# Optimization experiments

Hardware: AMD Instinct MI355X
Metric: run time of the kernel (lower is better)

The kernel has to match this reference:

```python
import jax, jax.numpy as jnp
import numpy as np

D = 512          # input_size (feature dim)
C = 100          # num_classes
N = 2048         # test samples
ALPHA = 0.5      # regularization mixing parameter
SHRINK = 1e-4    # shrinkage_param


def setup_inputs() -> dict:
    key = jax.random.key(0)
    k1, k2, k3, k4, k5 = jax.random.split(key, 5)
    X = jax.random.normal(k1, (N, D), dtype=jnp.float32)
    muK = jax.random.normal(k2, (C, D), dtype=jnp.float32)
    # Per-class covariances: PSD, well-conditioned (like fitted streaming covariances)
    A = jax.random.normal(k3, (C, D, D), dtype=jnp.float32) * 0.05
    SigmaK = jnp.einsum('cij,ckj->cik', A, A) + 0.1 * jnp.eye(D, dtype=jnp.float32)
    B = jax.random.normal(k4, (D, D), dtype=jnp.float32) * 0.05
    Sigma = B @ B.T + 0.1 * jnp.eye(D, dtype=jnp.float32)
    # class counts (all > 0 so every class is active)
    cK = jax.random.uniform(k5, (C,), dtype=jnp.float32, minval=1.0, maxval=1000.0)
    return {"X": X, "muK": muK, "SigmaK": SigmaK, "Sigma": Sigma, "cK": cK}


def reference(X, muK, SigmaK, Sigma, cK):
    # RegSigmaK[k] = alpha * SigmaK[k] + (1-alpha) * Sigma           [C, D, D]
    RegSigmaK = ALPHA * SigmaK + (1.0 - ALPHA) * Sigma[None, :, :]
    # priors (classes with zero count get prior 1, then are masked to -inf below)
    s = jnp.sum(cK)
    prior = jnp.where(cK == 0, 1.0, cK / s)                          # [C]
    # Lambda[k] = pinv((1-sh) * RegSigmaK[k] + sh * I)               [C, D, D]
    eye = jnp.eye(D, dtype=RegSigmaK.dtype)
    Lambda = jnp.linalg.pinv((1.0 - SHRINK) * RegSigmaK + SHRINK * eye)
    # 0.5 * log ||RegSigmaK[k]||_F  (torch.norm default = Frobenius)
    half_lognorm = 0.5 * jnp.log(jnp.linalg.norm(RegSigmaK, axis=(1, 2)))  # [C]
    # batched Mahalanobis quadratic form: (x - mu_k)^T Lambda_k (x - mu_k)
    diff = X[:, None, :] - muK[None, :, :]                           # [N, C, D]
    quad = jnp.einsum('ncd,cde,nce->nc', diff, Lambda, diff)         # [N, C]
    scores = jnp.log(prior)[None, :] - half_lognorm[None, :] - 0.5 * quad
    scores = jnp.where((cK == 0)[None, :], -jnp.inf, scores)
    return scores
```

## Files before the change

### kernel.cpp

```cpp
#include <hip/hip_runtime.h>
#include <math.h>

#define DIM 512
#define NCLS 100
#define NS 2048
#define DD (DIM*DIM)
#define SHRINKV 1e-4f

typedef short bf16x8 __attribute__((ext_vector_type(8)));
typedef short s16x4 __attribute__((ext_vector_type(4)));
typedef float f32x4 __attribute__((ext_vector_type(4)));

static __device__ __forceinline__ short f2bf(float f) {
  unsigned int u = __float_as_uint(f);
  u += 0x7FFFu + ((u >> 16) & 1u);
  return (short)(u >> 16);
}

__global__ __launch_bounds__(256) void prep_kernel(const float* __restrict__ SigmaK,
                                                   const float* __restrict__ Sigma,
                                                   float* __restrict__ M,
                                                   float* __restrict__ aux) {
  int b = blockIdx.x;
  int k = b >> 2, chunk = b & 3;
  const float* Sk = SigmaK + (size_t)k * DD;
  float* Mk = M + (size_t)k * DD;
  int base0 = chunk << 16;
  float fro = 0.f;
  const float oms = 1.0f - SHRINKV;
  for (int it = 0; it < 64; ++it) {
    int idx = base0 + (it << 10) + (threadIdx.x << 2);
    float4 a = *(const float4*)(Sk + idx);
    float4 g = *(const float4*)(Sigma + idx);
    int r = idx >> 9, c = idx & 511;
    float4 reg;
    reg.x = 0.5f*(a.x + g.x); reg.y = 0.5f*(a.y + g.y);
    reg.z = 0.5f*(a.z + g.z); reg.w = 0.5f*(a.w + g.w);
    fro += reg.x*reg.x + reg.y*reg.y + reg.z*reg.z + reg.w*reg.w;
    float4 m;
    m.x = oms*reg.x + ((r == c + 0) ? SHRINKV : 0.f);
    m.y = oms*reg.y + ((r == c + 1) ? SHRINKV : 0.f);
    m.z = oms*reg.z + ((r == c + 2) ? SHRINKV : 0.f);
    m.w = oms*reg.w + ((r == c + 3) ? SHRINKV : 0.f);
    *(float4*)(Mk + idx) = m;
  }
  __shared__ float red[4];
  int lane = threadIdx.x & 63, w = threadIdx.x >> 6;
  for (int o = 32; o > 0; o >>= 1) fro += __shfl_down(fro, o);
  if (lane == 0) red[w] = fro;
  __syncthreads();
  if (threadIdx.x == 0) atomicAdd(&aux[1 + k], red[0] + red[1] + red[2] + red[3]);
}

__global__ __launch_bounds__(256) void fdt_kernel(float* __restrict__ M,
                                                  short* __restrict__ Wb, int p) {
  __shared__ float Llds[64 * 68];
  __shared__ float invT[64 * 68];
  __shared__ float TA[64 * 68];
  int kcls = blockIdx.x;
  float* Mk = M + (size_t)kcls * DD;
  short* Wk = Wb + (size_t)kcls * DD;
  int tid = threadIdx.x, lane = tid & 63, wv = tid >> 6;
  int ty = tid >> 4, tx = tid & 15;
  int sr = tid >> 2, sq = (tid & 3) << 4;
  int p0 = p << 6;
  if (wv == 0) {
    float row[64];
    const float* src = Mk + (size_t)(p0 + lane) * DIM + p0;
    #pragma unroll
    for (int c4 = 0; c4 < 64; c4 += 4) {
      float4 v = *(const float4*)(src + c4);
      row[c4] = v.x; row[c4+1] = v.y; row[c4+2] = v.z; row[c4+3] = v.w;
    }
    #pragma unroll
    for (int j = 0; j < 64; ++j) {
      float diagv = __shfl(row[j], j);
      float dv = sqrtf(diagv);
      float rinv = 1.0f / dv;
      float myLj = row[j] * rinv;
      row[j] = myLj;
      #pragma unroll
      for (int c = j + 1; c < 64; ++c)
        row[c] = fmaf(-myLj, __shfl(myLj, c), row[c]);
    }
    #pragma unroll
    for (int c = 0; c < 64; ++c)
      Llds[lane * 68 + c] = (c <= lane) ? row[c] : 0.f;
  }
  __syncthreads();
  if (wv == 0) {
    float w[64];
    #pragma unroll
    for (int r = 0; r < 64; ++r) {
      float s = 0.f;
      #pragma unroll
      for (int kk = 0; kk + 4 <= r; kk += 4) {
        float4 lv = *(const float4*)(Llds + r*68 + kk);
        s += lv.x*w[kk] + lv.y*w[kk+1] + lv.z*w[kk+2] + lv.w*w[kk+3];
      }
      #pragma unroll
      for (int kk = r & ~3; kk < r; ++kk) s += Llds[r*68 + kk] * w[kk];
      float rhs = ((r == lane) ? 1.0f : 0.0f) - s;
      w[r] = rhs / Llds[r*68 + r];
    }
    #pragma unroll
    for (int r = 0; r < 64; ++r) {
      Mk[(size_t)(p0 + r)*DIM + p0 + lane] = w[r];
      Wk[(size_t)(p0 + r)*DIM + p0 + lane] = f2bf(w[r]);
      invT[lane*68 + r] = w[r];
    }
  }
  __syncthreads();
  for (int i = p + 1; i < 8; ++i) {
    {
      const float* a = Mk + (size_t)((i << 6) + sr)*DIM + p0 + sq;
      #pragma unroll
      for (int t4 = 0; t4 < 4; ++t4) {
        float4 va = *(const float4*)(a + 4*t4);
        TA[(sq+4*t4+0)*68+sr]=va.x; TA[(sq+4*t4+1)*68+sr]=va.y;
        TA[(sq+4*t4+2)*68+sr]=va.z; TA[(sq+4*t4+3)*68+sr]=va.w;
      }
    }
    __syncthreads();
    float acc[4][4];
    #pragma unroll
    for (int a2 = 0; a2 < 4; ++a2)
      #pragma unroll
      for (int b2 = 0; b2 < 4; ++b2) acc[a2][b2] = 0.f;
    #pragma unroll 16
    for (int m = 0; m < 64; ++m) {
      float4 av = *(const float4*)(TA + m*68 + (ty << 2));
      float4 bv = *(const float4*)(invT + m*68 + (tx << 2));
      float a4[4] = {av.x, av.y, av.z, av.w};
      float b4[4] = {bv.x, bv.y, bv.z, bv.w};
      #pragma unroll
      for (int ir = 0; ir < 4; ++ir)
        #pragma unroll
        for (int ic = 0; ic < 4; ++ic) acc[ir][ic] += a4[ir] * b4[ic];
    }
    #pragma unroll
    for (int q = 0; q < 4; ++q) {
      float4 v; v.x = acc[q][0]; v.y = acc[q][1]; v.z = acc[q][2]; v.w = acc[q][3];
      *(float4*)(Mk + (size_t)((i << 6) + (ty << 2) + q)*DIM + p0 + (tx << 2)) = v;
    }
    __syncthreads();
  }
}

__global__ __launch_bounds__(256) void syrk_kernel(float* __restrict__ M, int p) {
  __shared__ float TA[64 * 68];
  __shared__ float TB[64 * 68];
  int n = 7 - p;
  int T = n * (n + 1) / 2;
  int cls = blockIdx.x / T;
  int t = blockIdx.x % T;
  int bi = 0;
  while (t > bi) { t -= bi + 1; ++bi; }
  int i = p + 1 + bi, j = p + 1 + t;
  float* Mk = M + (size_t)cls * DD;
  int tid = threadIdx.x;
  int ty = tid >> 4, tx = tid & 15;
  int sr = tid >> 2, sq = (tid & 3) << 4;
  {
    const float* a = Mk + (size_t)((i << 6) + sr)*DIM + (p << 6) + sq;
    const float* b = Mk + (size_t)((j << 6) + sr)*DIM + (p << 6) + sq;
    #pragma unroll
    for (int t4 = 0; t4 < 4; ++t4) {
      float4 va = *(const float4*)(a + 4*t4);
      TA[(sq+4*t4+0)*68+sr]=va.x; TA[(sq+4*t4+1)*68+sr]=va.y;
      TA[(sq+4*t4+2)*68+sr]=va.z; TA[(sq+4*t4+3)*68+sr]=va.w;
      float4 vb = *(const float4*)(b + 4*t4);
      TB[(sq+4*t4+0)*68+sr]=vb.x; TB[(sq+4*t4+1)*68+sr]=vb.y;
      TB[(sq+4*t4+2)*68+sr]=vb.z; TB[(sq+4*t4+3)*68+sr]=vb.w;
    }
  }
  __syncthreads();
  float acc[4][4];
  #pragma unroll
  for (int a = 0; a < 4; ++a)
    #pragma unroll
    for (int b = 0; b < 4; ++b) acc[a][b] = 0.f;
  #pragma unroll 16
  for (int m = 0; m < 64; ++m) {
    float4 av = *(const float4*)(TA + m*68 + (ty << 2));
    float4 bv = *(const float4*)(TB + m*68 + (tx << 2));
    float a4[4] = {av.x, av.y, av.z, av.w};
    float b4[4] = {bv.x, bv.y, bv.z, bv.w};
    #pragma unroll
    for (int ir = 0; ir < 4; ++ir)
      #pragma unroll
      for (int ic = 0; ic < 4; ++ic) acc[ir][ic] += a4[ir] * b4[ic];
  }
  #pragma unroll
  for (int q = 0; q < 4; ++q) {
    float* dst = Mk + (size_t)((i << 6) + (ty << 2) + q)*DIM + (j << 6) + (tx << 2);
    float4 v = *(const float4*)dst;
    v.x -= acc[q][0]; v.y -= acc[q][1]; v.z -= acc[q][2]; v.w -= acc[q][3];
    *(float4*)dst = v;
  }
}

__global__ __launch_bounds__(256) void tail_kernel(float* __restrict__ M,
                                                   short* __restrict__ Wb) {
  __shared__ float Llds[64 * 68];
  __shared__ float invT[64 * 68];
  __shared__ float TA[64 * 68];
  __shared__ float TB[64 * 68];
  int kcls = blockIdx.x;
  float* Mk = M + (size_t)kcls * DD;
  short* Wk = Wb + (size_t)kcls * DD;
  int tid = threadIdx.x, lane = tid & 63, wv = tid >> 6;
  int ty = tid >> 4, tx = tid & 15;
  int sr = tid >> 2, sq = (tid & 3) << 4;
  for (int p = 4; p < 8; ++p) {
    int p0 = p << 6;
    __syncthreads();
    if (wv == 0) {
      float row[64];
      const float* src = Mk + (size_t)(p0 + lane) * DIM + p0;
      #pragma unroll
      for (int c4 = 0; c4 < 64; c4 += 4) {
        float4 v = *(const float4*)(src + c4);
        row[c4] = v.x; row[c4+1] = v.y; row[c4+2] = v.z; row[c4+3] = v.w;
      }
      #pragma unroll
      for (int j = 0; j < 64; ++j) {
        float diagv = __shfl(row[j], j);
        float dv = sqrtf(diagv);
        float rinv = 1.0f / dv;
        float myLj = row[j] * rinv;
        row[j] = myLj;
        #pragma unroll
        for (int c = j + 1; c < 64; ++c)
          row[c] = fmaf(-myLj, __shfl(myLj, c), row[c]);
      }
      #pragma unroll
      for (int c = 0; c < 64; ++c)
        Llds[lane * 68 + c] = (c <= lane) ? row[c] : 0.f;
    }
    __syncthreads();
    if (wv == 0) {
      float w[64];
      #pragma unroll
      for (int r = 0; r < 64; ++r) {
        float s = 0.f;
        #pragma unroll
        for (int kk = 0; kk + 4 <= r; kk += 4) {
          float4 lv = *(const float4*)(Llds + r*68 + kk);
          s += lv.x*w[kk] + lv.y*w[kk+1] + lv.z*w[kk+2] + lv.w*w[kk+3];
        }
        #pragma unroll
        for (int kk = r & ~3; kk < r; ++kk) s += Llds[r*68 + kk] * w[kk];
        float rhs = ((r == lane) ? 1.0f : 0.0f) - s;
        w[r] = rhs / Llds[r*68 + r];
      }
      #pragma unroll
      for (int r = 0; r < 64; ++r) {
        Mk[(size_t)(p0 + r)*DIM + p0 + lane] = w[r];
        Wk[(size_t)(p0 + r)*DIM + p0 + lane] = f2bf(w[r]);
        invT[lane*68 + r] = w[r];
      }
    }
    __syncthreads();
    for (int i = p + 1; i < 8; ++i) {
      {
        const float* a = Mk + (size_t)((i << 6) + sr)*DIM + p0 + sq;
        #pragma unroll
        for (int t4 = 0; t4 < 4; ++t4) {
          float4 va = *(const float4*)(a + 4*t4);
          TA[(sq+4*t4+0)*68+sr]=va.x; TA[(sq+4*t4+1)*68+sr]=va.y;
          TA[(sq+4*t4+2)*68+sr]=va.z; TA[(sq+4*t4+3)*68+sr]=va.w;
        }
      }
      __syncthreads();
      float acc[4][4];
      #pragma unroll
      for (int a2 = 0; a2 < 4; ++a2)
        #pragma unroll
        for (int b2 = 0; b2 < 4; ++b2) acc[a2][b2] = 0.f;
      #pragma unroll 16
      for (int m = 0; m < 64; ++m) {
        float4 av = *(const float4*)(TA + m*68 + (ty << 2));
        float4 bv = *(const float4*)(invT + m*68 + (tx << 2));
        float a4[4] = {av.x, av.y, av.z, av.w};
        float b4[4] = {bv.x, bv.y, bv.z, bv.w};
        #pragma unroll
        for (int ir = 0; ir < 4; ++ir)
          #pragma unroll
          for (int ic = 0; ic < 4; ++ic) acc[ir][ic] += a4[ir] * b4[ic];
      }
      #pragma unroll
      for (int q = 0; q < 4; ++q) {
        float4 v; v.x = acc[q][0]; v.y = acc[q][1]; v.z = acc[q][2]; v.w = acc[q][3];
        *(float4*)(Mk + (size_t)((i << 6) + (ty << 2) + q)*DIM + p0 + (tx << 2)) = v;
      }
      __syncthreads();
    }
    for (int i = p + 1; i < 8; ++i) {
      for (int j = p + 1; j <= i; ++j) {
        {
          const float* a = Mk + (size_t)((i << 6) + sr)*DIM + p0 + sq;
          const float* b = Mk + (size_t)((j << 6) + sr)*DIM + p0 + sq;
          #pragma unroll
          for (int t4 = 0; t4 < 4; ++t4) {
            float4 va = *(const float4*)(a + 4*t4);
            TA[(sq+4*t4+0)*68+sr]=va.x; TA[(sq+4*t4+1)*68+sr]=va.y;
            TA[(sq+4*t4+2)*68+sr]=va.z; TA[(sq+4*t4+3)*68+sr]=va.w;
            float4 vb = *(const float4*)(b + 4*t4);
            TB[(sq+4*t4+0)*68+sr]=vb.x; TB[(sq+4*t4+1)*68+sr]=vb.y;
            TB[(sq+4*t4+2)*68+sr]=vb.z; TB[(sq+4*t4+3)*68+sr]=vb.w;
          }
        }
        __syncthreads();
        float acc[4][4];
        #pragma unroll
        for (int a2 = 0; a2 < 4; ++a2)
          #pragma unroll
          for (int b2 = 0; b2 < 4; ++b2) acc[a2][b2] = 0.f;
        #pragma unroll 16
        for (int m = 0; m < 64; ++m) {
          float4 av = *(const float4*)(TA + m*68 + (ty << 2));
          float4 bv = *(const float4*)(TB + m*68 + (tx << 2));
          float a4[4] = {av.x, av.y, av.z, av.w};
          float b4[4] = {bv.x, bv.y, bv.z, bv.w};
          #pragma unroll
          for (int ir = 0; ir < 4; ++ir)
            #pragma unroll
            for (int ic = 0; ic < 4; ++ic) acc[ir][ic] += a4[ir] * b4[ic];
        }
        #pragma unroll
        for (int q = 0; q < 4; ++q) {
          float* dst = Mk + (size_t)((i << 6) + (ty << 2) + q)*DIM + (j << 6) + (tx << 2);
          float4 v = *(const float4*)dst;
          v.x -= acc[q][0]; v.y -= acc[q][1]; v.z -= acc[q][2]; v.w -= acc[q][3];
          *(float4*)dst = v;
        }
        __syncthreads();
      }
    }
  }
}

__global__ __launch_bounds__(256) void colsweep_kernel(float* __restrict__ M,
                                                       short* __restrict__ Wb) {
  __shared__ float TL[64 * 68];
  __shared__ float TW[64 * 68];
  int cls = blockIdx.x / 7;
  int j = blockIdx.x % 7;
  float* Mk = M + (size_t)cls * DD;
  short* Wk = Wb + (size_t)cls * DD;
  int tid = threadIdx.x;
  int ty = tid >> 4, tx = tid & 15;
  int sr = tid >> 2, sq = (tid & 3) << 4;
  for (int i = j + 1; i < 8; ++i) {
    float acc[4][4];
    #pragma unroll
    for (int a = 0; a < 4; ++a)
      #pragma unroll
      for (int b = 0; b < 4; ++b) acc[a][b] = 0.f;
    for (int k = j; k < i; ++k) {
      __syncthreads();
      {
        const float* a = Mk + (size_t)((i << 6) + sr)*DIM + (k << 6) + sq;
        const float* b = Mk + (size_t)((j << 6) + sr)*DIM + (k << 6) + sq;
        #pragma unroll
        for (int t4 = 0; t4 < 4; ++t4) {
          float4 va = *(const float4*)(a + 4*t4);
          TL[(sq+4*t4+0)*68+sr]=va.x; TL[(sq+4*t4+1)*68+sr]=va.y;
          TL[(sq+4*t4+2)*68+sr]=va.z; TL[(sq+4*t4+3)*68+sr]=va.w;
          *(float4*)(TW + sr*68 + sq + 4*t4) = *(const float4*)(b + 4*t4);
        }
      }
      __syncthreads();
      #pragma unroll 16
      for (int m = 0; m < 64; ++m) {
        float4 av = *(const float4*)(TL + m*68 + (ty << 2));
        float4 bv = *(const float4*)(TW + m*68 + (tx << 2));
        float a4[4] = {av.x, av.y, av.z, av.w};
        float b4[4] = {bv.x, bv.y, bv.z, bv.w};
        #pragma unroll
        for (int ir = 0; ir < 4; ++ir)
          #pragma unroll
          for (int ic = 0; ic < 4; ++ic) acc[ir][ic] += a4[ir] * b4[ic];
      }
    }
    __syncthreads();
    #pragma unroll
    for (int q = 0; q < 4; ++q) {
      float4 v; v.x = acc[q][0]; v.y = acc[q][1]; v.z = acc[q][2]; v.w = acc[q][3];
      *(float4*)(TW + ((ty << 2) + q)*68 + (tx << 2)) = v;
    }
    {
      const float* a = Mk + (size_t)((i << 6) + sr)*DIM + (i << 6) + sq;
      #pragma unroll
      for (int t4 = 0; t4 < 4; ++t4) {
        float4 va = *(const float4*)(a + 4*t4);
        TL[(sq+4*t4+0)*68+sr]=va.x; TL[(sq+4*t4+1)*68+sr]=va.y;
        TL[(sq+4*t4+2)*68+sr]=va.z; TL[(sq+4*t4+3)*68+sr]=va.w;
      }
    }
    __syncthreads();
    float r2[4][4];
    #pragma unroll
    for (int a = 0; a < 4; ++a)
      #pragma unroll
      for (int b = 0; b < 4; ++b) r2[a][b] = 0.f;
    #pragma unroll 16
    for (int m = 0; m < 64; ++m) {
      float4 av = *(const float4*)(TL + m*68 + (ty << 2));
      float4 bv = *(const float4*)(TW + m*68 + (tx << 2));
      float a4[4] = {av.x, av.y, av.z, av.w};
      float b4[4] = {bv.x, bv.y, bv.z, bv.w};
      #pragma unroll
      for (int ir = 0; ir < 4; ++ir)
        #pragma unroll
        for (int ic = 0; ic < 4; ++ic) r2[ir][ic] += a4[ir] * b4[ic];
    }
    #pragma unroll
    for (int q = 0; q < 4; ++q) {
      int a = (ty << 2) + q;
      float4 v; v.x = -r2[q][0]; v.y = -r2[q][1]; v.z = -r2[q][2]; v.w = -r2[q][3];
      *(float4*)(Mk + (size_t)((j << 6) + a)*DIM + (i << 6) + (tx << 2)) = v;
      s16x4 h;
      h[0] = f2bf(v.x); h[1] = f2bf(v.y); h[2] = f2bf(v.z); h[3] = f2bf(v.w);
      *(s16x4*)(Wk + (size_t)((i << 6) + a)*DIM + (j << 6) + (tx << 2)) = h;
    }
  }
}

__global__ __launch_bounds__(256) void score_kernel(const float* __restrict__ X,
                                                    const float* __restrict__ muK,
                                                    const float* __restrict__ cK,
                                                    const short* __restrict__ W,
                                                    const float* __restrict__ aux,
                                                    float* __restrict__ out) {
  __shared__ __align__(16) char WB4[4][8192];
  __shared__ float sred[4];
  int bid = blockIdx.x;
  int wg = ((bid & 7) * 400) + (bid >> 3);
  int kc = wg >> 5;
  int n0 = (wg & 31) << 6;
  int tid = threadIdx.x;
  int lane = tid & 63, wv = tid >> 6;
  const short* Wk = W + (size_t)kc * DD;
  const float* mu = muK + (size_t)kc * DIM;
  int r16 = lane & 15;
  int k8 = (lane >> 4) << 3;
  int arow = (wv << 4) + r16;

  int lrow = lane >> 3;
  int lcolel = ((lane & 7) ^ lrow) << 3;

  constexpr int SJT[36] = {0,1,1, 2,3,2,3,2,3,3, 4,5,4,5,4,5,4,5,4,5,5,
                           6,7,6,7,6,7,6,7,6,7,6,7,6,7,7};
  constexpr int SDC[36] = {0,0,1, 0,0,1,1,2,2,3, 0,0,1,1,2,2,3,3,4,4,5,
                           0,0,1,1,2,2,3,3,4,4,5,5,6,6,7};

  bf16x8 af[8][2];
  #pragma unroll
  for (int dc = 0; dc < 8; ++dc) {
    #pragma unroll
    for (int ks = 0; ks < 2; ++ks) {
      int col = (dc << 6) + (ks << 5) + k8;
      const float* xp = X + (size_t)(n0 + arow)*DIM + col;
      float4 x0 = *(const float4*)xp;
      float4 x1 = *(const float4*)(xp + 4);
      float4 m0 = *(const float4*)(mu + col);
      float4 m1 = *(const float4*)(mu + col + 4);
      bf16x8 h;
      h[0]=f2bf(x0.x-m0.x); h[1]=f2bf(x0.y-m0.y); h[2]=f2bf(x0.z-m0.z); h[3]=f2bf(x0.w-m0.w);
      h[4]=f2bf(x1.x-m1.x); h[5]=f2bf(x1.y-m1.y); h[6]=f2bf(x1.z-m1.z); h[7]=f2bf(x1.w-m1.w);
      af[dc][ks] = h;
    }
  }

  auto issue = [&](int s) {
    const int b = s & 3;
    const int rbase = SJT[s] << 6;
    const int cc = (SDC[s] << 6) + lcolel;
    #pragma unroll
    for (int q = 0; q < 2; ++q) {
      const short* g = Wk + (size_t)(rbase + (q << 5) + (wv << 3) + lrow)*DIM + cc;
      __builtin_amdgcn_global_load_lds(
          (const __attribute__((address_space(1))) void*)g,
          (__attribute__((address_space(3))) void*)(WB4[b] + (q << 12) + (wv << 10)),
          16, 0, 0);
    }
  };

  float qp[4] = {0.f, 0.f, 0.f, 0.f};
  f32x4 acc[2][4];
  #pragma unroll
  for (int a = 0; a < 2; ++a)
    #pragma unroll
    for (int jj = 0; jj < 4; ++jj) { acc[a][jj][0]=0.f; acc[a][jj][1]=0.f; acc[a][jj][2]=0.f; acc[a][jj][3]=0.f; }

  issue(0);
  issue(1);
  #pragma unroll
  for (int s = 0; s < 36; ++s) {
    const int jt = SJT[s], dc = SDC[s];
    if (s + 2 < 36) issue(s + 2);
    if (s < 34)      asm volatile("s_waitcnt vmcnt(4)" ::: "memory");
    else if (s == 34) asm volatile("s_waitcnt vmcnt(2)" ::: "memory");
    else              asm volatile("s_waitcnt vmcnt(0)" ::: "memory");
    __builtin_amdgcn_s_barrier();
    __builtin_amdgcn_sched_barrier(0);
    __builtin_amdgcn_s_setprio(1);
    #pragma unroll
    for (int ks = 0; ks < 2; ++ks) {
      #pragma unroll
      for (int jj = 0; jj < 4; ++jj) {
        int brow = (jj << 4) + r16;
        bf16x8 bfr = *(const bf16x8*)((const char*)WB4[s & 3] +
                     (((brow << 7) + (((ks << 5) + k8) << 1)) ^ ((brow & 7) << 4)));
        acc[jt & 1][jj] = __builtin_amdgcn_mfma_f32_16x16x32_bf16(af[dc][ks], bfr, acc[jt & 1][jj], 0, 0, 0);
      }
    }
    __builtin_amdgcn_s_setprio(0);
    if (s == 2 || s == 9 || s == 20 || s == 35) {
      #pragma unroll
      for (int a = 0; a < 2; ++a)
        #pragma unroll
        for (int jj = 0; jj < 4; ++jj)
          #pragma unroll
          for (int r = 0; r < 4; ++r) {
            float y = acc[a][jj][r]; qp[r] += y * y;
            acc[a][jj][r] = 0.f;
          }
    }
  }
  #pragma unroll
  for (int r = 0; r < 4; ++r) {
    qp[r] += __shfl_xor(qp[r], 1);
    qp[r] += __shfl_xor(qp[r], 2);
    qp[r] += __shfl_xor(qp[r], 4);
    qp[r] += __shfl_xor(qp[r], 8);
  }
  {
    float v = (tid < NCLS) ? cK[tid] : 0.f;
    #pragma unroll
    for (int o = 32; o > 0; o >>= 1) v += __shfl_xor(v, o);
    if (lane == 0) sred[wv] = v;
  }
  __syncthreads();
  float sumck = sred[0] + sred[1] + sred[2] + sred[3];
  float ck = cK[kc];
  float base;
  if (ck == 0.f) base = -INFINITY;
  else base = logf(ck) - logf(sumck) - 0.25f * logf(aux[1 + kc]);
  if ((lane & 15) == 0) {
    int nbase = n0 + (wv << 4) + ((lane >> 4) << 2);
    #pragma unroll
    for (int r = 0; r < 4; ++r)
      out[(size_t)(nbase + r)*NCLS + kc] = base - 0.5f * qp[r];
  }
}

extern "C" void kernel_launch(void* const* d_in, const int* in_sizes, int n_in,
                              void* d_out, int out_size, void* d_ws, size_t ws_size,
                              hipStream_t stream) {
  (void)in_sizes; (void)n_in; (void)out_size; (void)ws_size;
  const float* X      = (const float*)d_in[0];
  const float* muK    = (const float*)d_in[1];
  const float* SigmaK = (const float*)d_in[2];
  const float* Sigma  = (const float*)d_in[3];
  const float* cK     = (const float*)d_in[4];
  float* out = (float*)d_out;
  char* ws = (char*)d_ws;
  float* M   = (float*)ws;
  short* W   = (short*)(ws + (size_t)NCLS * DD * 4);
  float* aux = (float*)(ws + (size_t)NCLS * DD * 6);

  hipMemsetAsync(aux, 0, (1 + NCLS) * sizeof(float), stream);
  prep_kernel<<<400, 256, 0, stream>>>(SigmaK, Sigma, M, aux);
  for (int p = 0; p < 4; ++p) {
    fdt_kernel<<<NCLS, 256, 0, stream>>>(M, W, p);
    int n = 7 - p;
    syrk_kernel<<<NCLS * (n * (n + 1) / 2), 256, 0, stream>>>(M, p);
  }
  tail_kernel<<<NCLS, 256, 0, stream>>>(M, W);
  colsweep_kernel<<<NCLS * 7, 256, 0, stream>>>(M, W);
  score_kernel<<<NCLS * 32, 256, 0, stream>>>(X, muK, cK, W, aux, out);
}
```

Before: 879.6 us.

## Replace serial tail kernel with per-panel launches and double-buffer LDS staging

Removes the single-block-per-class tail_kernel that serially ran the last four Cholesky panels, and instead runs fdt and syrk launches for all eight panels so the trailing updates spread across many blocks. The fdt kernel now double-buffers the TA tile, and its idle waves preload the first row-block while wave 0 factors the diagonal. Colsweep also double-buffers its TL/TW tiles, prefetching the next k-block while computing the current one. This adds more kernel launches and doubles LDS use, which may lower occupancy.

```diff
diff --git a/kernel.cpp b/kernel.cpp
--- a/kernel.cpp
+++ b/kernel.cpp
@@ -56,7 +56,7 @@
                                                   short* __restrict__ Wb, int p) {
   __shared__ float Llds[64 * 68];
   __shared__ float invT[64 * 68];
-  __shared__ float TA[64 * 68];
+  __shared__ float TA[2][64 * 68];
   int kcls = blockIdx.x;
   float* Mk = M + (size_t)kcls * DD;
   short* Wk = Wb + (size_t)kcls * DD;
@@ -109,19 +109,26 @@
       Wk[(size_t)(p0 + r)*DIM + p0 + lane] = f2bf(w[r]);
       invT[lane*68 + r] = w[r];
     }
+  } else if (p < 7) {
+    int w1 = wv - 1;
+    int r0 = (w1 == 0) ? 0 : (w1 == 1 ? 22 : 43);
+    int r1 = (w1 == 0) ? 22 : (w1 == 1 ? 43 : 64);
+    const float* ab = Mk + ((size_t)((p + 1) << 6)) * DIM + p0;
+    for (int row = r0; row < r1; ++row)
+      TA[0][lane*68 + row] = ab[(size_t)row * DIM + lane];
   }
   __syncthreads();
+  int cur = 0;
   for (int i = p + 1; i < 8; ++i) {
-    {
-      const float* a = Mk + (size_t)((i << 6) + sr)*DIM + p0 + sq;
+    if (i + 1 < 8) {
+      const float* a = Mk + (size_t)(((i + 1) << 6) + sr)*DIM + p0 + sq;
       #pragma unroll
       for (int t4 = 0; t4 < 4; ++t4) {
         float4 va = *(const float4*)(a + 4*t4);
-        TA[(sq+4*t4+0)*68+sr]=va.x; TA[(sq+4*t4+1)*68+sr]=va.y;
-        TA[(sq+4*t4+2)*68+sr]=va.z; TA[(sq+4*t4+3)*68+sr]=va.w;
-      }
-    }
-    __syncthreads();
+        TA[cur^1][(sq+4*t4+0)*68+sr]=va.x; TA[cur^1][(sq+4*t4+1)*68+sr]=va.y;
+        TA[cur^1][(sq+4*t4+2)*68+sr]=va.z; TA[cur^1][(sq+4*t4+3)*68+sr]=va.w;
+      }
+    }
     float acc[4][4];
     #pragma unroll
     for (int a2 = 0; a2 < 4; ++a2)
@@ -129,7 +136,7 @@
       for (int b2 = 0; b2 < 4; ++b2) acc[a2][b2] = 0.f;
     #pragma unroll 16
     for (int m = 0; m < 64; ++m) {
-      float4 av = *(const float4*)(TA + m*68 + (ty << 2));
+      float4 av = *(const float4*)(TA[cur] + m*68 + (ty << 2));
       float4 bv = *(const float4*)(invT + m*68 + (tx << 2));
       float a4[4] = {av.x, av.y, av.z, av.w};
       float b4[4] = {bv.x, bv.y, bv.z, bv.w};
@@ -144,6 +151,7 @@
       *(float4*)(Mk + (size_t)((i << 6) + (ty << 2) + q)*DIM + p0 + (tx << 2)) = v;
     }
     __syncthreads();
+    cur ^= 1;
   }
 }
 
@@ -200,151 +208,10 @@
   }
 }
 
-__global__ __launch_bounds__(256) void tail_kernel(float* __restrict__ M,
-                                                   short* __restrict__ Wb) {
-  __shared__ float Llds[64 * 68];
-  __shared__ float invT[64 * 68];
-  __shared__ float TA[64 * 68];
-  __shared__ float TB[64 * 68];
-  int kcls = blockIdx.x;
-  float* Mk = M + (size_t)kcls * DD;
-  short* Wk = Wb + (size_t)kcls * DD;
-  int tid = threadIdx.x, lane = tid & 63, wv = tid >> 6;
-  int ty = tid >> 4, tx = tid & 15;
-  int sr = tid >> 2, sq = (tid & 3) << 4;
-  for (int p = 4; p < 8; ++p) {
-    int p0 = p << 6;
-    __syncthreads();
-    if (wv == 0) {
-      float row[64];
-      const float* src = Mk + (size_t)(p0 + lane) * DIM + p0;
-      #pragma unroll
-      for (int c4 = 0; c4 < 64; c4 += 4) {
-        float4 v = *(const float4*)(src + c4);
-        row[c4] = v.x; row[c4+1] = v.y; row[c4+2] = v.z; row[c4+3] = v.w;
-      }
-      #pragma unroll
-      for (int j = 0; j < 64; ++j) {
-        float diagv = __shfl(row[j], j);
-        float dv = sqrtf(diagv);
-        float rinv = 1.0f / dv;
-        float myLj = row[j] * rinv;
-        row[j] = myLj;
-        #pragma unroll
-        for (int c = j + 1; c < 64; ++c)
-          row[c] = fmaf(-myLj, __shfl(myLj, c), row[c]);
-      }
-      #pragma unroll
-      for (int c = 0; c < 64; ++c)
-        Llds[lane * 68 + c] = (c <= lane) ? row[c] : 0.f;
-    }
-    __syncthreads();
-    if (wv == 0) {
-      float w[64];
-      #pragma unroll
-      for (int r = 0; r < 64; ++r) {
-        float s = 0.f;
-        #pragma unroll
-        for (int kk = 0; kk + 4 <= r; kk += 4) {
-          float4 lv = *(const float4*)(Llds + r*68 + kk);
-          s += lv.x*w[kk] + lv.y*w[kk+1] + lv.z*w[kk+2] + lv.w*w[kk+3];
-        }
-        #pragma unroll
-        for (int kk = r & ~3; kk < r; ++kk) s += Llds[r*68 + kk] * w[kk];
-        float rhs = ((r == lane) ? 1.0f : 0.0f) - s;
-        w[r] = rhs / Llds[r*68 + r];
-      }
-      #pragma unroll
-      for (int r = 0; r < 64; ++r) {
-        Mk[(size_t)(p0 + r)*DIM + p0 + lane] = w[r];
-        Wk[(size_t)(p0 + r)*DIM + p0 + lane] = f2bf(w[r]);
-        invT[lane*68 + r] = w[r];
-      }
-    }
-    __syncthreads();
-    for (int i = p + 1; i < 8; ++i) {
-      {
-        const float* a = Mk + (size_t)((i << 6) + sr)*DIM + p0 + sq;
-        #pragma unroll
-        for (int t4 = 0; t4 < 4; ++t4) {
-          float4 va = *(const float4*)(a + 4*t4);
-          TA[(sq+4*t4+0)*68+sr]=va.x; TA[(sq+4*t4+1)*68+sr]=va.y;
-          TA[(sq+4*t4+2)*68+sr]=va.z; TA[(sq+4*t4+3)*68+sr]=va.w;
-        }
-      }
-      __syncthreads();
-      float acc[4][4];
-      #pragma unroll
-      for (int a2 = 0; a2 < 4; ++a2)
-        #pragma unroll
-        for (int b2 = 0; b2 < 4; ++b2) acc[a2][b2] = 0.f;
-      #pragma unroll 16
-      for (int m = 0; m < 64; ++m) {
-        float4 av = *(const float4*)(TA + m*68 + (ty << 2));
-        float4 bv = *(const float4*)(invT + m*68 + (tx << 2));
-        float a4[4] = {av.x, av.y, av.z, av.w};
-        float b4[4] = {bv.x, bv.y, bv.z, bv.w};
-        #pragma unroll
-        for (int ir = 0; ir < 4; ++ir)
-          #pragma unroll
-          for (int ic = 0; ic < 4; ++ic) acc[ir][ic] += a4[ir] * b4[ic];
-      }
-      #pragma unroll
-      for (int q = 0; q < 4; ++q) {
-        float4 v; v.x = acc[q][0]; v.y = acc[q][1]; v.z = acc[q][2]; v.w = acc[q][3];
-        *(float4*)(Mk + (size_t)((i << 6) + (ty << 2) + q)*DIM + p0 + (tx << 2)) = v;
-      }
-      __syncthreads();
-    }
-    for (int i = p + 1; i < 8; ++i) {
-      for (int j = p + 1; j <= i; ++j) {
-        {
-          const float* a = Mk + (size_t)((i << 6) + sr)*DIM + p0 + sq;
-          const float* b = Mk + (size_t)((j << 6) + sr)*DIM + p0 + sq;
-          #pragma unroll
-          for (int t4 = 0; t4 < 4; ++t4) {
-            float4 va = *(const float4*)(a + 4*t4);
-            TA[(sq+4*t4+0)*68+sr]=va.x; TA[(sq+4*t4+1)*68+sr]=va.y;
-            TA[(sq+4*t4+2)*68+sr]=va.z; TA[(sq+4*t4+3)*68+sr]=va.w;
-            float4 vb = *(const float4*)(b + 4*t4);
-            TB[(sq+4*t4+0)*68+sr]=vb.x; TB[(sq+4*t4+1)*68+sr]=vb.y;
-            TB[(sq+4*t4+2)*68+sr]=vb.z; TB[(sq+4*t4+3)*68+sr]=vb.w;
-          }
-        }
-        __syncthreads();
-        float acc[4][4];
-        #pragma unroll
-        for (int a2 = 0; a2 < 4; ++a2)
-          #pragma unroll
-          for (int b2 = 0; b2 < 4; ++b2) acc[a2][b2] = 0.f;
-        #pragma unroll 16
-        for (int m = 0; m < 64; ++m) {
-          float4 av = *(const float4*)(TA + m*68 + (ty << 2));
-          float4 bv = *(const float4*)(TB + m*68 + (tx << 2));
-          float a4[4] = {av.x, av.y, av.z, av.w};
-          float b4[4] = {bv.x, bv.y, bv.z, bv.w};
-          #pragma unroll
-          for (int ir = 0; ir < 4; ++ir)
-            #pragma unroll
-            for (int ic = 0; ic < 4; ++ic) acc[ir][ic] += a4[ir] * b4[ic];
-        }
-        #pragma unroll
-        for (int q = 0; q < 4; ++q) {
-          float* dst = Mk + (size_t)((i << 6) + (ty << 2) + q)*DIM + (j << 6) + (tx << 2);
-          float4 v = *(const float4*)dst;
-          v.x -= acc[q][0]; v.y -= acc[q][1]; v.z -= acc[q][2]; v.w -= acc[q][3];
-          *(float4*)dst = v;
-        }
-        __syncthreads();
-      }
-    }
-  }
-}
-
 __global__ __launch_bounds__(256) void colsweep_kernel(float* __restrict__ M,
                                                        short* __restrict__ Wb) {
-  __shared__ float TL[64 * 68];
-  __shared__ float TW[64 * 68];
+  __shared__ float TL[2][64 * 68];
+  __shared__ float TW[2][64 * 68];
   int cls = blockIdx.x / 7;
   int j = blockIdx.x % 7;
   float* Mk = M + (size_t)cls * DD;
@@ -353,29 +220,31 @@
   int ty = tid >> 4, tx = tid & 15;
   int sr = tid >> 2, sq = (tid & 3) << 4;
   for (int i = j + 1; i < 8; ++i) {
+    auto stageLW = [&](int k, int buf) {
+      const float* a = Mk + (size_t)((i << 6) + sr)*DIM + (k << 6) + sq;
+      const float* b = Mk + (size_t)((j << 6) + sr)*DIM + (k << 6) + sq;
+      #pragma unroll
+      for (int t4 = 0; t4 < 4; ++t4) {
+        float4 va = *(const float4*)(a + 4*t4);
+        TL[buf][(sq+4*t4+0)*68+sr]=va.x; TL[buf][(sq+4*t4+1)*68+sr]=va.y;
+        TL[buf][(sq+4*t4+2)*68+sr]=va.z; TL[buf][(sq+4*t4+3)*68+sr]=va.w;
+        *(float4*)(TW[buf] + sr*68 + sq + 4*t4) = *(const float4*)(b + 4*t4);
+      }
+    };
     float acc[4][4];
     #pragma unroll
     for (int a = 0; a < 4; ++a)
       #pragma unroll
       for (int b = 0; b < 4; ++b) acc[a][b] = 0.f;
+    stageLW(j, 0);
+    __syncthreads();
+    int cur = 0;
     for (int k = j; k < i; ++k) {
-      __syncthreads();
-      {
-        const float* a = Mk + (size_t)((i << 6) + sr)*DIM + (k << 6) + sq;
-        const float* b = Mk + (size_t)((j << 6) + sr)*DIM + (k << 6) + sq;
-        #pragma unroll
-        for (int t4 = 0; t4 < 4; ++t4) {
-          float4 va = *(const float4*)(a + 4*t4);
-          TL[(sq+4*t4+0)*68+sr]=va.x; TL[(sq+4*t4+1)*68+sr]=va.y;
-          TL[(sq+4*t4+2)*68+sr]=va.z; TL[(sq+4*t4+3)*68+sr]=va.w;
-          *(float4*)(TW + sr*68 + sq + 4*t4) = *(const float4*)(b + 4*t4);
-        }
-      }
-      __syncthreads();
+      if (k + 1 < i) stageLW(k + 1, cur ^ 1);
       #pragma unroll 16
       for (int m = 0; m < 64; ++m) {
-        float4 av = *(const float4*)(TL + m*68 + (ty << 2));
-        float4 bv = *(const float4*)(TW + m*68 + (tx << 2));
+        float4 av = *(const float4*)(TL[cur] + m*68 + (ty << 2));
+        float4 bv = *(const float4*)(TW[cur] + m*68 + (tx << 2));
         float a4[4] = {av.x, av.y, av.z, av.w};
         float b4[4] = {bv.x, bv.y, bv.z, bv.w};
         #pragma unroll
@@ -383,20 +252,21 @@
           #pragma unroll
           for (int ic = 0; ic < 4; ++ic) acc[ir][ic] += a4[ir] * b4[ic];
       }
-    }
-    __syncthreads();
+      __syncthreads();
+      cur ^= 1;
+    }
     #pragma unroll
     for (int q = 0; q < 4; ++q) {
       float4 v; v.x = acc[q][0]; v.y = acc[q][1]; v.z = acc[q][2]; v.w = acc[q][3];
-      *(float4*)(TW + ((ty << 2) + q)*68 + (tx << 2)) = v;
+      *(float4*)(TW[0] + ((ty << 2) + q)*68 + (tx << 2)) = v;
     }
     {
       const float* a = Mk + (size_t)((i << 6) + sr)*DIM + (i << 6) + sq;
       #pragma unroll
       for (int t4 = 0; t4 < 4; ++t4) {
         float4 va = *(const float4*)(a + 4*t4);
-        TL[(sq+4*t4+0)*68+sr]=va.x; TL[(sq+4*t4+1)*68+sr]=va.y;
-        TL[(sq+4*t4+2)*68+sr]=va.z; TL[(sq+4*t4+3)*68+sr]=va.w;
+        TL[0][(sq+4*t4+0)*68+sr]=va.x; TL[0][(sq+4*t4+1)*68+sr]=va.y;
+        TL[0][(sq+4*t4+2)*68+sr]=va.z; TL[0][(sq+4*t4+3)*68+sr]=va.w;
       }
     }
     __syncthreads();
@@ -407,8 +277,8 @@
       for (int b = 0; b < 4; ++b) r2[a][b] = 0.f;
     #pragma unroll 16
     for (int m = 0; m < 64; ++m) {
-      float4 av = *(const float4*)(TL + m*68 + (ty << 2));
-      float4 bv = *(const float4*)(TW + m*68 + (tx << 2));
+      float4 av = *(const float4*)(TL[0] + m*68 + (ty << 2));
+      float4 bv = *(const float4*)(TW[0] + m*68 + (tx << 2));
       float a4[4] = {av.x, av.y, av.z, av.w};
       float b4[4] = {bv.x, bv.y, bv.z, bv.w};
       #pragma unroll
@@ -425,6 +295,7 @@
       h[0] = f2bf(v.x); h[1] = f2bf(v.y); h[2] = f2bf(v.z); h[3] = f2bf(v.w);
       *(s16x4*)(Wk + (size_t)((i << 6) + a)*DIM + (j << 6) + (tx << 2)) = h;
     }
+    __syncthreads();
   }
 }
 
@@ -574,12 +445,11 @@
 
   hipMemsetAsync(aux, 0, (1 + NCLS) * sizeof(float), stream);
   prep_kernel<<<400, 256, 0, stream>>>(SigmaK, Sigma, M, aux);
-  for (int p = 0; p < 4; ++p) {
+  for (int p = 0; p < 8; ++p) {
     fdt_kernel<<<NCLS, 256, 0, stream>>>(M, W, p);
     int n = 7 - p;
-    syrk_kernel<<<NCLS * (n * (n + 1) / 2), 256, 0, stream>>>(M, p);
-  }
-  tail_kernel<<<NCLS, 256, 0, stream>>>(M, W);
+    if (n > 0) syrk_kernel<<<NCLS * (n * (n + 1) / 2), 256, 0, stream>>>(M, p);
+  }
   colsweep_kernel<<<NCLS * 7, 256, 0, stream>>>(M, W);
   score_kernel<<<NCLS * 32, 256, 0, stream>>>(X, muK, cK, W, aux, out);
 }
```

Result: no change. 871.2 us (-1.0%).
